# Performance work log

Hardware: AMD Instinct MI355X
Metric: run time of the kernel (lower is better)

Reference implementation:

```python
import jax, jax.numpy as jnp
import numpy as np

N_NODES = 50000
N_EDGES = 800000
N_GRAPHS = 256


def setup_inputs() -> dict:
    key = jax.random.key(0)
    ks = jax.random.split(key, 20)
    s = 0.05
    return {
        "x": jax.random.normal(ks[0], (N_NODES, 128), jnp.float32),
        "edge_index": jax.random.randint(ks[1], (2, N_EDGES), 0, N_NODES, jnp.int64),
        "batch_index": jnp.sort(jax.random.randint(ks[2], (N_NODES,), 0, N_GRAPHS, jnp.int64)),
        "mol_features": jax.random.normal(ks[3], (N_GRAPHS, 256), jnp.float32),
        "gcn_W": jax.random.normal(ks[4], (3, 128, 128), jnp.float32) * s,
        "gcn_b": jax.random.normal(ks[5], (3, 128), jnp.float32) * s,
        "gcn_out_W": jax.random.normal(ks[6], (128, 128), jnp.float32) * s,
        "gcn_out_b": jax.random.normal(ks[7], (128,), jnp.float32) * s,
        "mlp_W": jax.random.normal(ks[8], (2, 256, 256), jnp.float32) * s,
        "mlp_b": jax.random.normal(ks[9], (2, 256), jnp.float32) * s,
        "mlp_out_W": jax.random.normal(ks[10], (64, 256), jnp.float32) * s,
        "mlp_out_b": jax.random.normal(ks[11], (64,), jnp.float32) * s,
        "pred_W1": jax.random.normal(ks[12], (256, 192), jnp.float32) * s,
        "pred_b1": jax.random.normal(ks[13], (256,), jnp.float32) * s,
        "pred_W2": jax.random.normal(ks[14], (256, 256), jnp.float32) * s,
        "pred_b2": jax.random.normal(ks[15], (256,), jnp.float32) * s,
        "out_W": jax.random.normal(ks[16], (1, 256), jnp.float32) * s,
        "out_b": jax.random.normal(ks[17], (1,), jnp.float32) * s,
    }


def reference(x, edge_index, batch_index, mol_features,
              gcn_W, gcn_b, gcn_out_W, gcn_out_b,
              mlp_W, mlp_b, mlp_out_W, mlp_out_b,
              pred_W1, pred_b1, pred_W2, pred_b2, out_W, out_b):
    N = x.shape[0]
    E = edge_index.shape[1]
    G = mol_features.shape[0]
    row, col = edge_index[0], edge_index[1]

    # GCN normalization with self-loops (PyG gcn_norm, symmetric):
    # deg[i] = in-degree(i) + 1 (self loop); norm_e = d^-1/2[row] * d^-1/2[col]
    deg = jax.ops.segment_sum(jnp.ones((E,), x.dtype), col, num_segments=N) + 1.0
    dinv = jax.lax.rsqrt(deg)
    enorm = (dinv[row] * dinv[col])[:, None]     # [E,1]
    self_c = (dinv * dinv)[:, None]              # [N,1] self-loop coefficient

    h1 = x
    for i in range(gcn_W.shape[0]):
        h = h1 @ gcn_W[i].T                      # per-node transform [N,128]
        agg = jax.ops.segment_sum(h[row] * enorm, col, num_segments=N)
        h1 = jax.nn.relu(agg + self_c * h + gcn_b[i])
    h1 = h1 @ gcn_out_W.T + gcn_out_b            # final GCN-branch Linear (no relu)

    # global_mean_pool over batch_index -> [G,128]
    sums = jax.ops.segment_sum(h1, batch_index, num_segments=G)
    counts = jax.ops.segment_sum(jnp.ones((N,), x.dtype), batch_index, num_segments=G)
    h1 = sums / jnp.maximum(counts, 1.0)[:, None]

    # MLP branch: relu after every linear (including last)
    h2 = mol_features
    for i in range(mlp_W.shape[0]):
        h2 = jax.nn.relu(h2 @ mlp_W[i].T + mlp_b[i])
    h2 = jax.nn.relu(h2 @ mlp_out_W.T + mlp_out_b)

    h = jnp.concatenate([h1, h2], axis=1)        # [G,192]
    h = jax.nn.relu(h @ pred_W1.T + pred_b1)
    h = jax.nn.relu(h @ pred_W2.T + pred_b2)
    return h @ out_W.T + out_b                   # [G,1]
```

## Files before the change

kernel.cpp:

```cpp
#include <hip/hip_runtime.h>


typedef __attribute__((ext_vector_type(8))) short short8;
typedef __attribute__((ext_vector_type(4))) float f32x4;

#define BKT 64
#define SL 16
#define CAP 192
#define WCAP 2560
#define NBINBLK 2048
#define HROWS 65536

#define HW_MLP0 0
#define HW_MLP1 65536
#define HW_MLO  131072
#define HW_GCNO 147456
#define HW_PW1  163840
#define HW_PW2  212992
#define HW_TOT  278528

__device__ __forceinline__ unsigned short f2bf(float f) {
    union { float f; unsigned u; } c; c.f = f;
    unsigned u = c.u;
    unsigned r = u + 0x7FFFu + ((u >> 16) & 1u);
    return (unsigned short)(r >> 16);
}
__device__ __forceinline__ float bflo(unsigned w) {
    union { unsigned u; float f; } c; c.u = w << 16; return c.f;
}
__device__ __forceinline__ float bfhi(unsigned w) {
    union { unsigned u; float f; } c; c.u = w & 0xFFFF0000u; return c.f;
}

__global__ void k_init(int* cur, float* pool, float* cnt,
                       const float* __restrict__ gcnW, uint4* __restrict__ Wb,
                       const float* __restrict__ mlpW, const float* __restrict__ mloW,
                       const float* __restrict__ gcnoW, const float* __restrict__ pW1,
                       const float* __restrict__ pW2, unsigned short* __restrict__ Wh,
                       unsigned short* xb, unsigned short* bufA, unsigned short* bufB,
                       const int* __restrict__ batch, int M, int G, int N) {
    int i = blockIdx.x * 256 + threadIdx.x;
    if (i < M * 16) cur[i] = 0;
    if (i < G * 128) pool[i] = 0.f;
    if (i < G) {
        int lo = 0, hi = N;
        while (lo < hi) { int m = (lo + hi) >> 1; if (batch[m] < i) lo = m + 1; else hi = m; }
        int lo2 = lo, hi2 = N;
        while (lo2 < hi2) { int m = (lo2 + hi2) >> 1; if (batch[m] < i + 1) lo2 = m + 1; else hi2 = m; }
        cnt[i] = (float)(lo2 - lo);
    }
    if (i < 192) {
        unsigned short* b = (i < 64) ? xb : (i < 128) ? bufA : bufB;
        *(unsigned*)(b + (size_t)N * 128 + (i & 63) * 2) = 0u;
    }
    if (i < 3 * 2048) {
        int l = i >> 11, rem = i & 2047;
        int o = rem >> 4, c = rem & 15;
        const float4* s = (const float4*)(gcnW + (size_t)l * 16384 + o * 128 + c * 8);
        float4 a = s[0], b = s[1];
        uint4 v;
        v.x = ((unsigned)f2bf(a.y) << 16) | f2bf(a.x);
        v.y = ((unsigned)f2bf(a.w) << 16) | f2bf(a.z);
        v.z = ((unsigned)f2bf(b.y) << 16) | f2bf(b.x);
        v.w = ((unsigned)f2bf(b.w) << 16) | f2bf(b.z);
        Wb[(l << 11) | (o << 4) | (c ^ (o & 15))] = v;
    }
    int j = i - 8192;
    if (j >= 0 && j < (HW_TOT / 8)) {
        int e = j * 8;
        const float* src;
        if (e < HW_MLO)        src = mlpW  + e;
        else if (e < HW_GCNO)  src = mloW  + (e - HW_MLO);
        else if (e < HW_PW1)   src = gcnoW + (e - HW_GCNO);
        else if (e < HW_PW2)   src = pW1   + (e - HW_PW1);
        else                   src = pW2   + (e - HW_PW2);
        float4 a = *(const float4*)src;
        float4 b = *((const float4*)src + 1);
        uint4 v;
        v.x = ((unsigned)f2bf(a.y) << 16) | f2bf(a.x);
        v.y = ((unsigned)f2bf(a.w) << 16) | f2bf(a.z);
        v.z = ((unsigned)f2bf(b.y) << 16) | f2bf(b.x);
        v.w = ((unsigned)f2bf(b.w) << 16) | f2bf(b.z);
        *(uint4*)(Wh + e) = v;
    }
}

__global__ __launch_bounds__(256) void k_bin(const int* __restrict__ row,
                                             const int* __restrict__ col,
                                             int* __restrict__ cur,
                                             unsigned* __restrict__ gbin,
                                             int E, int C) {
    const int x = blockIdx.x & (SL - 1);
    int e0 = blockIdx.x * C, e1 = min(E, e0 + C);
    for (int e = e0 + threadIdx.x; e < e1; e += 256) {
        int c = col[e];
        int cell = (c >> 6) * SL + x;
        int cnt = atomicAdd(&cur[cell << 4], 1);
        gbin[cell * CAP + cnt] = (unsigned)row[e] | ((unsigned)(c & 63) << 16);
    }
}

__global__ __launch_bounds__(256) void k_csr(const unsigned* __restrict__ gbin,
                                             const int* __restrict__ cur,
                                             int* __restrict__ rs,
                                             unsigned short* __restrict__ rd,
                                             float* __restrict__ dinv,
                                             unsigned short* __restrict__ csrf,
                                             const float* __restrict__ x,
                                             unsigned short* __restrict__ xb,
                                             int N) {
    const int b = blockIdx.x, t = threadIdx.x;
    __shared__ int hcnt[64], lcur[64], fills[SL];
    __shared__ float sdinv[64];
    if (t < 64) hcnt[t] = 0;
    if (t < SL) fills[t] = cur[(b * SL + t) << 4];
    __syncthreads();
    #pragma unroll 4
    for (int xx = 0; xx < SL; ++xx) {
        int cbase = (b * SL + xx) * CAP, fill = fills[xx];
        for (int i = t; i < fill; i += 256)
            atomicAdd(&hcnt[(gbin[cbase + i] >> 16) & 63], 1);
    }
    __syncthreads();
    if (t < 64) {
        int v = hcnt[t];
        int vp = (v + 7) & ~7;
        int xs = vp;
        #pragma unroll
        for (int off = 1; off < 64; off <<= 1) {
            int u = __shfl_up(xs, off, 64);
            if (t >= off) xs += u;
        }
        int excl = xs - vp;
        lcur[t] = excl;
        float d = rsqrtf((float)v + 1.0f);
        sdinv[t] = d;
        int node = b * 64 + t;
        rs[node] = b * WCAP + excl;
        rd[node] = (unsigned short)v;
        dinv[node] = d;
    }
    __syncthreads();
    #pragma unroll 4
    for (int xx = 0; xx < SL; ++xx) {
        int cbase = (b * SL + xx) * CAP, fill = fills[xx];
        for (int i = t; i < fill; i += 256) {
            unsigned v = gbin[cbase + i];
            int p = atomicAdd(&lcur[(v >> 16) & 63], 1);
            csrf[b * WCAP + p] = (unsigned short)(v & 0xFFFFu);
        }
    }
    __syncthreads();
    if (t < 64) {
        int v = hcnt[t], vp = (v + 7) & ~7;
        int base = lcur[t];
        for (int p = v; p < vp; ++p)
            csrf[b * WCAP + base + (p - v)] = (unsigned short)N;
    }
    const int node0 = b * 64;
    #pragma unroll
    for (int it = 0; it < 4; ++it) {
        int i = t + it * 256;
        int nd = node0 + (i >> 4);
        if (nd < N) {
            int ch = i & 15;
            float d = sdinv[i >> 4];
            const float4* s = (const float4*)(x + (size_t)nd * 128 + ch * 8);
            float4 a = s[0], bb = s[1];
            uint4 o;
            o.x = ((unsigned)f2bf(d * a.y) << 16) | f2bf(d * a.x);
            o.y = ((unsigned)f2bf(d * a.w) << 16) | f2bf(d * a.z);
            o.z = ((unsigned)f2bf(d * bb.y) << 16) | f2bf(d * bb.x);
            o.w = ((unsigned)f2bf(d * bb.w) << 16) | f2bf(d * bb.z);
            *(uint4*)(xb + (size_t)nd * 128 + ch * 8) = o;
        }
    }
}

__global__ __launch_bounds__(1024, 8) void k_fused(
    const unsigned short* __restrict__ h,
    const uint4* __restrict__ Wb,
    const float* __restrict__ bias,
    const float* __restrict__ dscale,
    const float* __restrict__ dinv,
    const int* __restrict__ rs,
    const unsigned short* __restrict__ rd,
    const unsigned short* __restrict__ csrf,
    unsigned short* __restrict__ C,
    const int* __restrict__ batch,
    float* __restrict__ pool, int N) {
    __shared__ uint4 Wsh[2048];
    __shared__ unsigned short Ash[64][136];
    __shared__ unsigned short Ish[WCAP];

    const int t = threadIdx.x;
    Wsh[t] = Wb[t];
    Wsh[t + 1024] = Wb[t + 1024];

    const int sub = t >> 4;
    const int fg = t & 15;
    const int blk0 = blockIdx.x * 64;
    const int node = blk0 + sub;

    const int base = blockIdx.x * WCAP;
    const int ln = blk0 + 63;
    const int wcnt = (rs[ln] + ((rd[ln] + 7) & ~7)) - base;
    for (int i = t * 8; i < wcnt; i += 8192)
        *(uint4*)(&Ish[i]) = *(const uint4*)(csrf + base + i);
    __syncthreads();

    float acc[8] = {0.f, 0.f, 0.f, 0.f, 0.f, 0.f, 0.f, 0.f};
    const unsigned fgo = (unsigned)fg * 8u;
    if (node < N) {
        uint4 hv = *(const uint4*)(h + (size_t)node * 128u + fgo);
        acc[0] = bflo(hv.x); acc[1] = bfhi(hv.x);
        acc[2] = bflo(hv.y); acc[3] = bfhi(hv.y);
        acc[4] = bflo(hv.z); acc[5] = bfhi(hv.z);
        acc[6] = bflo(hv.w); acc[7] = bfhi(hv.w);
    }
    {
        const int stl = rs[node] - base;
        const int epl = stl + ((rd[node] + 7) & ~7);
        #pragma unroll 1
        for (int i = stl; i < epl; i += 4) {
            const uint2 iv = *(const uint2*)(&Ish[i]);
            const uint4 v0 = *(const uint4*)(h + ((iv.x & 0xFFFFu) * 128u + fgo));
            const uint4 v1 = *(const uint4*)(h + ((iv.x >> 16)     * 128u + fgo));
            const uint4 v2 = *(const uint4*)(h + ((iv.y & 0xFFFFu) * 128u + fgo));
            const uint4 v3 = *(const uint4*)(h + ((iv.y >> 16)     * 128u + fgo));
            acc[0] += bflo(v0.x); acc[1] += bfhi(v0.x);
            acc[2] += bflo(v0.y); acc[3] += bfhi(v0.y);
            acc[4] += bflo(v0.z); acc[5] += bfhi(v0.z);
            acc[6] += bflo(v0.w); acc[7] += bfhi(v0.w);
            acc[0] += bflo(v1.x); acc[1] += bfhi(v1.x);
            acc[2] += bflo(v1.y); acc[3] += bfhi(v1.y);
            acc[4] += bflo(v1.z); acc[5] += bfhi(v1.z);
            acc[6] += bflo(v1.w); acc[7] += bfhi(v1.w);
            acc[0] += bflo(v2.x); acc[1] += bfhi(v2.x);
            acc[2] += bflo(v2.y); acc[3] += bfhi(v2.y);
            acc[4] += bflo(v2.z); acc[5] += bfhi(v2.z);
            acc[6] += bflo(v2.w); acc[7] += bfhi(v2.w);
            acc[0] += bflo(v3.x); acc[1] += bfhi(v3.x);
            acc[2] += bflo(v3.y); acc[3] += bfhi(v3.y);
            acc[4] += bflo(v3.z); acc[5] += bfhi(v3.z);
            acc[6] += bflo(v3.w); acc[7] += bfhi(v3.w);
        }
    }
    {
        const float dn = (node < N) ? dinv[node] : 0.f;
        unsigned short ob[8];
        #pragma unroll
        for (int j = 0; j < 8; ++j) ob[j] = f2bf(acc[j] * dn);
        uint4 o;
        o.x = ((unsigned)ob[1] << 16) | ob[0];
        o.y = ((unsigned)ob[3] << 16) | ob[2];
        o.z = ((unsigned)ob[5] << 16) | ob[4];
        o.w = ((unsigned)ob[7] << 16) | ob[6];
        *(uint4*)(&Ash[sub][fg * 8]) = o;
    }
    __syncthreads();

    const int lane = t & 63;
    const int wv = t >> 6;
    const int l15 = lane & 15, quad = lane >> 4;
    const int rt = wv & 3, cp = wv >> 2;
    f32x4 acc2[2];
    acc2[0] = (f32x4){0.f, 0.f, 0.f, 0.f};
    acc2[1] = (f32x4){0.f, 0.f, 0.f, 0.f};
    #pragma unroll
    for (int kiter = 0; kiter < 4; ++kiter) {
        short8 af = *(const short8*)(&Ash[rt * 16 + l15][kiter * 32 + quad * 8]);
        const int cswz = (kiter * 4 + quad) ^ l15;
        #pragma unroll
        for (int cc = 0; cc < 2; ++cc) {
            int ct = cp * 2 + cc;
            short8 bf = *(const short8*)(&Wsh[((ct * 16 + l15) << 4) | cswz]);
            acc2[cc] = __builtin_amdgcn_mfma_f32_16x16x32_bf16(af, bf, acc2[cc], 0, 0, 0);
        }
    }

    const int rbase = blk0 + rt * 16 + quad * 4;
    if (pool) {
        int gr[4];
        #pragma unroll
        for (int r = 0; r < 4; ++r)
            gr[r] = (rbase + r < N) ? batch[rbase + r] : -1;
        #pragma unroll
        for (int cc = 0; cc < 2; ++cc) {
            int colc = (cp * 2 + cc) * 16 + l15;
            float bcol = bias[colc];
            float s = 0.f; int gprev = -2;
            #pragma unroll
            for (int r = 0; r < 4; ++r) {
                if (gr[r] >= 0) {
                    float v = fmaxf(acc2[cc][r] + bcol, 0.f);
                    if (gr[r] == gprev) s += v;
                    else {
                        if (gprev >= 0) atomicAdd(&pool[(size_t)gprev * 128 + colc], s);
                        gprev = gr[r]; s = v;
                    }
                }
            }
            if (gprev >= 0) atomicAdd(&pool[(size_t)gprev * 128 + colc], s);
        }
    } else {
        float ds[4];
        #pragma unroll
        for (int r = 0; r < 4; ++r) {
            int rr = rbase + r;
            ds[r] = (dscale && rr < N) ? dscale[rr] : 1.f;
        }
        #pragma unroll
        for (int cc = 0; cc < 2; ++cc) {
            int colc = (cp * 2 + cc) * 16 + l15;
            float bcol = bias[colc];
            #pragma unroll
            for (int r = 0; r < 4; ++r) {
                int rr = rbase + r;
                if (rr < N) {
                    float v = fmaxf(acc2[cc][r] + bcol, 0.f) * ds[r];
                    C[(size_t)rr * 128 + colc] = f2bf(v);
                }
            }
        }
    }
}

__global__ __launch_bounds__(256) void k_head(
    const unsigned short* __restrict__ Wh,
    const float* __restrict__ pool, const float* __restrict__ cnt,
    const float* __restrict__ mol,
    const float* __restrict__ mlpb, const float* __restrict__ mlob,
    const float* __restrict__ gcnob,
    const float* __restrict__ pb1, const float* __restrict__ pb2,
    const float* __restrict__ oW, const float* __restrict__ ob,
    float* __restrict__ out, int G) {
    const int g0 = blockIdx.x * 16;
    const int t = threadIdx.x;
    const int lane = t & 63, wv = t >> 6;
    const int l15 = lane & 15, quad = lane >> 4;
    __shared__ unsigned short A[16][264], B[16][264], Cc[16][200], Mn[16][136];
    __shared__ float red[4][16];

    for (int i = t; i < 16 * 256; i += 256) {
        int g = i >> 8, k = i & 255;
        A[g][k] = f2bf(mol[(size_t)(g0 + g) * 256 + k]);
    }
    for (int i = t; i < 16 * 128; i += 256) {
        int g = i >> 7, k = i & 127;
        float c = cnt[g0 + g];
        Mn[g][k] = f2bf(pool[(size_t)(g0 + g) * 128 + k] / fmaxf(c, 1.f));
    }
    __syncthreads();

    auto do_tile = [&](const unsigned short* actb, int astr, int K,
                       const unsigned short* W, int orow,
                       const float* __restrict__ bias, int bidx,
                       unsigned short* dstb, int dstr, int ocol, bool dorelu) {
        f32x4 c = {0.f, 0.f, 0.f, 0.f};
        for (int kt = 0; kt < (K >> 5); ++kt) {
            short8 af = *(const short8*)(actb + (size_t)l15 * astr + kt * 32 + quad * 8);
            short8 bf = *(const short8*)(W + (size_t)orow * K + kt * 32 + quad * 8);
            c = __builtin_amdgcn_mfma_f32_16x16x32_bf16(af, bf, c, 0, 0, 0);
        }
        float bb = bias[bidx];
        #pragma unroll
        for (int r = 0; r < 4; ++r) {
            int g = quad * 4 + r;
            float v = c[r] + bb;
            if (dorelu) v = fmaxf(v, 0.f);
            dstb[(size_t)g * dstr + ocol] = f2bf(v);
        }
    };

    #pragma unroll
    for (int nt = 0; nt < 4; ++nt) {
        int o = (wv * 4 + nt) * 16 + l15;
        do_tile(&A[0][0], 264, 256, Wh + HW_MLP0, o, mlpb, o, &B[0][0], 264, o, true);
    }
    __syncthreads();
    #pragma unroll
    for (int nt = 0; nt < 4; ++nt) {
        int o = (wv * 4 + nt) * 16 + l15;
        do_tile(&B[0][0], 264, 256, Wh + HW_MLP1, o, mlpb + 256, o, &A[0][0], 264, o, true);
    }
    __syncthreads();
    #pragma unroll
    for (int j = 0; j < 3; ++j) {
        int tile = wv * 3 + j;
        if (tile < 8) {
            int o = tile * 16 + l15;
            do_tile(&Mn[0][0], 136, 128, Wh + HW_GCNO, o, gcnob, o, &Cc[0][0], 200, o, false);
        } else {
            int om = (tile - 8) * 16 + l15;
            do_tile(&A[0][0], 264, 256, Wh + HW_MLO, om, mlob, om, &Cc[0][0], 200, 128 + om, true);
        }
    }
    __syncthreads();
    #pragma unroll
    for (int nt = 0; nt < 4; ++nt) {
        int o = (wv * 4 + nt) * 16 + l15;
        do_tile(&Cc[0][0], 200, 192, Wh + HW_PW1, o, pb1, o, &B[0][0], 264, o, true);
    }
    __syncthreads();
    {
        float pacc[4] = {0.f, 0.f, 0.f, 0.f};
        #pragma unroll
        for (int nt = 0; nt < 4; ++nt) {
            int o = (wv * 4 + nt) * 16 + l15;
            f32x4 c = {0.f, 0.f, 0.f, 0.f};
            #pragma unroll
            for (int kt = 0; kt < 8; ++kt) {
                short8 af = *(const short8*)(&B[0][0] + (size_t)l15 * 264 + kt * 32 + quad * 8);
                short8 bf = *(const short8*)(Wh + HW_PW2 + (size_t)o * 256 + kt * 32 + quad * 8);
                c = __builtin_amdgcn_mfma_f32_16x16x32_bf16(af, bf, c, 0, 0, 0);
            }
            float bb = pb2[o], wo = oW[o];
            #pragma unroll
            for (int r = 0; r < 4; ++r)
                pacc[r] += fmaxf(c[r] + bb, 0.f) * wo;
        }
        #pragma unroll
        for (int off = 1; off < 16; off <<= 1)
            #pragma unroll
            for (int r = 0; r < 4; ++r)
                pacc[r] += __shfl_xor(pacc[r], off, 64);
        if (l15 == 0) {
            #pragma unroll
            for (int r = 0; r < 4; ++r)
                red[wv][quad * 4 + r] = pacc[r];
        }
    }
    __syncthreads();
    if (t < 16) {
        float s = red[0][t] + red[1][t] + red[2][t] + red[3][t] + ob[0];
        if (g0 + t < G) out[g0 + t] = s;
    }
}

extern "C" void kernel_launch(void* const* d_in, const int* in_sizes, int n_in,
                              void* d_out, int out_size, void* d_ws, size_t ws_size,
                              hipStream_t stream) {
    const float* x     = (const float*)d_in[0];
    const int*   ei    = (const int*)d_in[1];
    const int*   batch = (const int*)d_in[2];
    const float* mol   = (const float*)d_in[3];
    const float* gcnW  = (const float*)d_in[4];
    const float* gcnb  = (const float*)d_in[5];
    const float* gcnoW = (const float*)d_in[6];
    const float* gcnob = (const float*)d_in[7];
    const float* mlpW  = (const float*)d_in[8];
    const float* mlpb  = (const float*)d_in[9];
    const float* mloW  = (const float*)d_in[10];
    const float* mlob  = (const float*)d_in[11];
    const float* pW1   = (const float*)d_in[12];
    const float* pb1   = (const float*)d_in[13];
    const float* pW2   = (const float*)d_in[14];
    const float* pb2   = (const float*)d_in[15];
    const float* oW    = (const float*)d_in[16];
    const float* ob    = (const float*)d_in[17];

    const int N = in_sizes[0] / 128;
    const int E = in_sizes[1] / 2;
    const int G = in_sizes[3] / 256;
    const int* row = ei;
    const int* col = ei + E;

    const int NBK = (N + BKT - 1) / BKT;
    const int M = NBK * SL;
    const int C = (E + NBINBLK - 1) / NBINBLK;

    char* p = (char*)d_ws;
    auto alloc = [&](size_t bytes) {
        char* q = p;
        p += (bytes + 255) & ~(size_t)255;
        return (void*)q;
    };
    int*    rs    = (int*)alloc((size_t)NBK * 64 * 4);
    unsigned short* rd = (unsigned short*)alloc((size_t)NBK * 64 * 2);
    float*  dinv  = (float*)alloc((size_t)NBK * 64 * 4);
    int*    cur   = (int*)alloc((size_t)M * 16 * 4);
    unsigned* gbin = (unsigned*)alloc((size_t)M * CAP * 4);
    unsigned short* csrf = (unsigned short*)alloc(((size_t)NBK * WCAP + 32) * 2);
    unsigned short* xb   = (unsigned short*)alloc((size_t)HROWS * 128 * 2);
    unsigned short* bufA = (unsigned short*)alloc((size_t)HROWS * 128 * 2);
    unsigned short* bufB = (unsigned short*)alloc((size_t)HROWS * 128 * 2);
    uint4*  Wb    = (uint4*)alloc((size_t)3 * 2048 * 16);
    unsigned short* Wh = (unsigned short*)alloc((size_t)HW_TOT * 2);
    float*  pool  = (float*)alloc((size_t)G * 128 * 4);
    float*  cnt   = (float*)alloc((size_t)G * 4);

    const int initblocks = (M * 16 + 255) / 256;

    k_init<<<initblocks, 256, 0, stream>>>(cur, pool, cnt, gcnW, Wb,
                                           mlpW, mloW, gcnoW, pW1, pW2, Wh,
                                           xb, bufA, bufB, batch, M, G, N);
    k_bin<<<NBINBLK, 256, 0, stream>>>(row, col, cur, gbin, E, C);
    k_csr<<<NBK, 256, 0, stream>>>(gbin, cur, rs, rd, dinv, csrf, x, xb, N);

    const int fblocks = (N + 63) / 64;
    k_fused<<<fblocks, 1024, 0, stream>>>(xb, Wb, gcnb, dinv, dinv,
                                          rs, rd, csrf, bufA,
                                          batch, (float*)nullptr, N);
    k_fused<<<fblocks, 1024, 0, stream>>>(bufA, Wb + 2048, gcnb + 128, dinv, dinv,
                                          rs, rd, csrf, bufB,
                                          batch, (float*)nullptr, N);
    k_fused<<<fblocks, 1024, 0, stream>>>(bufB, Wb + 4096, gcnb + 256,
                                          (const float*)nullptr, dinv,
                                          rs, rd, csrf, bufA,
                                          batch, pool, N);
    k_head<<<(G + 15) / 16, 256, 0, stream>>>(
        Wh, pool, cnt, mol, mlpb, mlob, gcnob, pb1, pb2, oW, ob,
        (float*)d_out, G);
}
```

Baseline: 320.8 us.

## Merge all stages into one persistent cooperative kernel with grid syncs

Replaces the seven separate launches (init, bin, csr, three GCN layers, head) with one cooperative persistent kernel. Stages are separated by grid-wide syncs, and each stage uses grid-stride loops over tiles. The goal is to remove launch overhead and the gaps between kernels. In exchange, grid syncs add cost, the grid is capped at a few hundred blocks of 1024 threads, and stages with little work (csr, head) leave most threads idle.

```diff
diff --git a/kernel.cpp b/kernel.cpp
--- a/kernel.cpp
+++ b/kernel.cpp
@@ -1,4 +1,6 @@
 #include <hip/hip_runtime.h>
+#include <hip/hip_cooperative_groups.h>
+namespace cg = cooperative_groups;
 
 
 typedef __attribute__((ext_vector_type(8))) short short8;
@@ -8,7 +10,6 @@
 #define SL 16
 #define CAP 192
 #define WCAP 2560
-#define NBINBLK 2048
 #define HROWS 65536
 
 #define HW_MLP0 0
@@ -32,409 +33,415 @@
     union { unsigned u; float f; } c; c.u = w & 0xFFFF0000u; return c.f;
 }
 
-__global__ void k_init(int* cur, float* pool, float* cnt,
-                       const float* __restrict__ gcnW, uint4* __restrict__ Wb,
-                       const float* __restrict__ mlpW, const float* __restrict__ mloW,
-                       const float* __restrict__ gcnoW, const float* __restrict__ pW1,
-                       const float* __restrict__ pW2, unsigned short* __restrict__ Wh,
-                       unsigned short* xb, unsigned short* bufA, unsigned short* bufB,
-                       const int* __restrict__ batch, int M, int G, int N) {
-    int i = blockIdx.x * 256 + threadIdx.x;
-    if (i < M * 16) cur[i] = 0;
-    if (i < G * 128) pool[i] = 0.f;
-    if (i < G) {
-        int lo = 0, hi = N;
-        while (lo < hi) { int m = (lo + hi) >> 1; if (batch[m] < i) lo = m + 1; else hi = m; }
-        int lo2 = lo, hi2 = N;
-        while (lo2 < hi2) { int m = (lo2 + hi2) >> 1; if (batch[m] < i + 1) lo2 = m + 1; else hi2 = m; }
-        cnt[i] = (float)(lo2 - lo);
+struct MegaParams {
+    int* cur; float* pool; float* cnt;
+    const float* gcnW; uint4* Wb;
+    const float* mlpW; const float* mloW; const float* gcnoW;
+    const float* pW1; const float* pW2; unsigned short* Wh;
+    unsigned short* xb; unsigned short* bufA; unsigned short* bufB;
+    const int* batch; const int* row; const int* col;
+    unsigned* gbin;
+    int* rs; unsigned short* rd; float* dinv; unsigned short* csrf;
+    const float* x; const float* gcnb;
+    const float* mol; const float* mlpb; const float* mlob; const float* gcnob;
+    const float* pb1; const float* pb2; const float* oW; const float* ob;
+    float* out;
+    int M, G, N, E, NBK;
+};
+
+__global__ __launch_bounds__(1024, 8) void k_mega(MegaParams p) {
+    cg::grid_group gg = cg::this_grid();
+    const int t = threadIdx.x;
+    const int nb = gridDim.x;
+
+    union SMem {
+        struct { uint4 Wsh[2048]; unsigned short Ash[64][136];
+                 unsigned short Ish[WCAP]; } f;
+        struct { int hcnt[64]; int lcur[64]; int fills[SL];
+                 float sdinv[64]; } c;
+        struct { unsigned short A[16][264]; unsigned short Bs[16][264];
+                 unsigned short Cc[16][200]; unsigned short Mn[16][136];
+                 float red[4][16]; } h;
+    };
+    __shared__ SMem sm;
+
+    {
+        const int itot = p.M * 16;
+        for (int i = blockIdx.x * 1024 + t; i < itot; i += nb * 1024) {
+            p.cur[i] = 0;
+            if (i < p.G * 128) p.pool[i] = 0.f;
+            if (i < p.G) {
+                int lo = 0, hi = p.N;
+                while (lo < hi) { int m = (lo + hi) >> 1; if (p.batch[m] < i) lo = m + 1; else hi = m; }
+                int lo2 = lo, hi2 = p.N;
+                while (lo2 < hi2) { int m = (lo2 + hi2) >> 1; if (p.batch[m] < i + 1) lo2 = m + 1; else hi2 = m; }
+                p.cnt[i] = (float)(lo2 - lo);
+            }
+            if (i < 192) {
+                unsigned short* b = (i < 64) ? p.xb : (i < 128) ? p.bufA : p.bufB;
+                *(unsigned*)(b + (size_t)p.N * 128 + (i & 63) * 2) = 0u;
+            }
+            if (i < 3 * 2048) {
+                int l = i >> 11, rem = i & 2047;
+                int o = rem >> 4, c = rem & 15;
+                const float4* s = (const float4*)(p.gcnW + (size_t)l * 16384 + o * 128 + c * 8);
+                float4 a = s[0], b = s[1];
+                uint4 v;
+                v.x = ((unsigned)f2bf(a.y) << 16) | f2bf(a.x);
+                v.y = ((unsigned)f2bf(a.w) << 16) | f2bf(a.z);
+                v.z = ((unsigned)f2bf(b.y) << 16) | f2bf(b.x);
+                v.w = ((unsigned)f2bf(b.w) << 16) | f2bf(b.z);
+                p.Wb[(l << 11) | (o << 4) | (c ^ (o & 15))] = v;
+            }
+            int j = i - 8192;
+            if (j >= 0 && j < (HW_TOT / 8)) {
+                int e = j * 8;
+                const float* src;
+                if (e < HW_MLO)        src = p.mlpW  + e;
+                else if (e < HW_GCNO)  src = p.mloW  + (e - HW_MLO);
+                else if (e < HW_PW1)   src = p.gcnoW + (e - HW_GCNO);
+                else if (e < HW_PW2)   src = p.pW1   + (e - HW_PW1);
+                else                   src = p.pW2   + (e - HW_PW2);
+                float4 a = *(const float4*)src;
+                float4 b = *((const float4*)src + 1);
+                uint4 v;
+                v.x = ((unsigned)f2bf(a.y) << 16) | f2bf(a.x);
+                v.y = ((unsigned)f2bf(a.w) << 16) | f2bf(a.z);
+                v.z = ((unsigned)f2bf(b.y) << 16) | f2bf(b.x);
+                v.w = ((unsigned)f2bf(b.w) << 16) | f2bf(b.z);
+                *(uint4*)(p.Wh + e) = v;
+            }
+        }
     }
-    if (i < 192) {
-        unsigned short* b = (i < 64) ? xb : (i < 128) ? bufA : bufB;
-        *(unsigned*)(b + (size_t)N * 128 + (i & 63) * 2) = 0u;
+    gg.sync();
+
+    {
+        const int x = blockIdx.x & (SL - 1);
+        for (int e = blockIdx.x * 1024 + t; e < p.E; e += nb * 1024) {
+            int c = p.col[e];
+            int cell = (c >> 6) * SL + x;
+            int cnt = atomicAdd(&p.cur[cell << 4], 1);
+            p.gbin[cell * CAP + cnt] = (unsigned)p.row[e] | ((unsigned)(c & 63) << 16);
+        }
     }
-    if (i < 3 * 2048) {
-        int l = i >> 11, rem = i & 2047;
-        int o = rem >> 4, c = rem & 15;
-        const float4* s = (const float4*)(gcnW + (size_t)l * 16384 + o * 128 + c * 8);
-        float4 a = s[0], b = s[1];
-        uint4 v;
-        v.x = ((unsigned)f2bf(a.y) << 16) | f2bf(a.x);
-        v.y = ((unsigned)f2bf(a.w) << 16) | f2bf(a.z);
-        v.z = ((unsigned)f2bf(b.y) << 16) | f2bf(b.x);
-        v.w = ((unsigned)f2bf(b.w) << 16) | f2bf(b.z);
-        Wb[(l << 11) | (o << 4) | (c ^ (o & 15))] = v;
+    gg.sync();
+
+    for (int b = blockIdx.x; b < p.NBK; b += nb) {
+        if (t < 64) sm.c.hcnt[t] = 0;
+        if (t < SL) sm.c.fills[t] = p.cur[(b * SL + t) << 4];
+        __syncthreads();
+        for (int xx = 0; xx < SL; ++xx) {
+            int cbase = (b * SL + xx) * CAP, fill = sm.c.fills[xx];
+            for (int i = t; i < fill; i += 1024)
+                atomicAdd(&sm.c.hcnt[(p.gbin[cbase + i] >> 16) & 63], 1);
+        }
+        __syncthreads();
+        if (t < 64) {
+            int v = sm.c.hcnt[t];
+            int vp = (v + 7) & ~7;
+            int xs = vp;
+            #pragma unroll
+            for (int off = 1; off < 64; off <<= 1) {
+                int u = __shfl_up(xs, off, 64);
+                if (t >= off) xs += u;
+            }
+            int excl = xs - vp;
+            sm.c.lcur[t] = excl;
+            float d = rsqrtf((float)v + 1.0f);
+            sm.c.sdinv[t] = d;
+            int node = b * 64 + t;
+            p.rs[node] = b * WCAP + excl;
+            p.rd[node] = (unsigned short)v;
+            p.dinv[node] = d;
+        }
+        __syncthreads();
+        for (int xx = 0; xx < SL; ++xx) {
+            int cbase = (b * SL + xx) * CAP, fill = sm.c.fills[xx];
+            for (int i = t; i < fill; i += 1024) {
+                unsigned v = p.gbin[cbase + i];
+                int pp = atomicAdd(&sm.c.lcur[(v >> 16) & 63], 1);
+                p.csrf[b * WCAP + pp] = (unsigned short)(v & 0xFFFFu);
+            }
+        }
+        __syncthreads();
+        if (t < 64) {
+            int v = sm.c.hcnt[t], vp = (v + 7) & ~7;
+            int base = sm.c.lcur[t];
+            for (int q = v; q < vp; ++q)
+                p.csrf[b * WCAP + base + (q - v)] = (unsigned short)p.N;
+        }
+        {
+            int nd = b * 64 + (t >> 4);
+            if (nd < p.N) {
+                int ch = t & 15;
+                float d = sm.c.sdinv[t >> 4];
+                const float4* s = (const float4*)(p.x + (size_t)nd * 128 + ch * 8);
+                float4 a = s[0], bb = s[1];
+                uint4 o;
+                o.x = ((unsigned)f2bf(d * a.y) << 16) | f2bf(d * a.x);
+                o.y = ((unsigned)f2bf(d * a.w) << 16) | f2bf(d * a.z);
+                o.z = ((unsigned)f2bf(d * bb.y) << 16) | f2bf(d * bb.x);
+                o.w = ((unsigned)f2bf(d * bb.w) << 16) | f2bf(d * bb.z);
+                *(uint4*)(p.xb + (size_t)nd * 128 + ch * 8) = o;
+            }
+        }
+        __syncthreads();
     }
-    int j = i - 8192;
-    if (j >= 0 && j < (HW_TOT / 8)) {
-        int e = j * 8;
-        const float* src;
-        if (e < HW_MLO)        src = mlpW  + e;
-        else if (e < HW_GCNO)  src = mloW  + (e - HW_MLO);
-        else if (e < HW_PW1)   src = gcnoW + (e - HW_GCNO);
-        else if (e < HW_PW2)   src = pW1   + (e - HW_PW1);
-        else                   src = pW2   + (e - HW_PW2);
-        float4 a = *(const float4*)src;
-        float4 b = *((const float4*)src + 1);
-        uint4 v;
-        v.x = ((unsigned)f2bf(a.y) << 16) | f2bf(a.x);
-        v.y = ((unsigned)f2bf(a.w) << 16) | f2bf(a.z);
-        v.z = ((unsigned)f2bf(b.y) << 16) | f2bf(b.x);
-        v.w = ((unsigned)f2bf(b.w) << 16) | f2bf(b.z);
-        *(uint4*)(Wh + e) = v;
+    gg.sync();
+
+    {
+        const int sub = t >> 4;
+        const int fg = t & 15;
+        const unsigned fgo = (unsigned)fg * 8u;
+        const int fblocks = (p.N + 63) / 64;
+        for (int l = 0; l < 3; ++l) {
+            const unsigned short* h = (l == 0) ? p.xb : (l == 1) ? p.bufA : p.bufB;
+            unsigned short* Cd = (l == 0) ? p.bufA : p.bufB;
+            const float* dscale = (l < 2) ? p.dinv : (const float*)nullptr;
+            float* pl = (l == 2) ? p.pool : (float*)nullptr;
+            const float* bias = p.gcnb + l * 128;
+            const uint4* Wbl = p.Wb + l * 2048;
+            sm.f.Wsh[t] = Wbl[t];
+            sm.f.Wsh[t + 1024] = Wbl[t + 1024];
+
+            for (int tile = blockIdx.x; tile < fblocks; tile += nb) {
+                __syncthreads();
+                const int blk0 = tile * 64;
+                const int node = blk0 + sub;
+                const int base = tile * WCAP;
+                const int ln = blk0 + 63;
+                const int wcnt = (p.rs[ln] + ((p.rd[ln] + 7) & ~7)) - base;
+                for (int i = t * 8; i < wcnt; i += 8192)
+                    *(uint4*)(&sm.f.Ish[i]) = *(const uint4*)(p.csrf + base + i);
+                __syncthreads();
+
+                float acc[8] = {0.f, 0.f, 0.f, 0.f, 0.f, 0.f, 0.f, 0.f};
+                if (node < p.N) {
+                    uint4 hv = *(const uint4*)(h + (size_t)node * 128u + fgo);
+                    acc[0] = bflo(hv.x); acc[1] = bfhi(hv.x);
+                    acc[2] = bflo(hv.y); acc[3] = bfhi(hv.y);
+                    acc[4] = bflo(hv.z); acc[5] = bfhi(hv.z);
+                    acc[6] = bflo(hv.w); acc[7] = bfhi(hv.w);
+                }
+                {
+                    const int stl = p.rs[node] - base;
+                    const int epl = stl + ((p.rd[node] + 7) & ~7);
+                    #pragma unroll 1
+                    for (int i = stl; i < epl; i += 4) {
+                        const uint2 iv = *(const uint2*)(&sm.f.Ish[i]);
+                        const uint4 v0 = *(const uint4*)(h + ((iv.x & 0xFFFFu) * 128u + fgo));
+                        const uint4 v1 = *(const uint4*)(h + ((iv.x >> 16)     * 128u + fgo));
+                        const uint4 v2 = *(const uint4*)(h + ((iv.y & 0xFFFFu) * 128u + fgo));
+                        const uint4 v3 = *(const uint4*)(h + ((iv.y >> 16)     * 128u + fgo));
+                        acc[0] += bflo(v0.x); acc[1] += bfhi(v0.x);
+                        acc[2] += bflo(v0.y); acc[3] += bfhi(v0.y);
+                        acc[4] += bflo(v0.z); acc[5] += bfhi(v0.z);
+                        acc[6] += bflo(v0.w); acc[7] += bfhi(v0.w);
+                        acc[0] += bflo(v1.x); acc[1] += bfhi(v1.x);
+                        acc[2] += bflo(v1.y); acc[3] += bfhi(v1.y);
+                        acc[4] += bflo(v1.z); acc[5] += bfhi(v1.z);
+                        acc[6] += bflo(v1.w); acc[7] += bfhi(v1.w);
+                        acc[0] += bflo(v2.x); acc[1] += bfhi(v2.x);
+                        acc[2] += bflo(v2.y); acc[3] += bfhi(v2.y);
+                        acc[4] += bflo(v2.z); acc[5] += bfhi(v2.z);
+                        acc[6] += bflo(v2.w); acc[7] += bfhi(v2.w);
+                        acc[0] += bflo(v3.x); acc[1] += bfhi(v3.x);
+                        acc[2] += bflo(v3.y); acc[3] += bfhi(v3.y);
+                        acc[4] += bflo(v3.z); acc[5] += bfhi(v3.z);
+                        acc[6] += bflo(v3.w); acc[7] += bfhi(v3.w);
+                    }
+                }
+                {
+                    const float dn = (node < p.N) ? p.dinv[node] : 0.f;
+                    unsigned short ob[8];
+                    #pragma unroll
+                    for (int j = 0; j < 8; ++j) ob[j] = f2bf(acc[j] * dn);
+                    uint4 o;
+                    o.x = ((unsigned)ob[1] << 16) | ob[0];
+                    o.y = ((unsigned)ob[3] << 16) | ob[2];
+                    o.z = ((unsigned)ob[5] << 16) | ob[4];
+                    o.w = ((unsigned)ob[7] << 16) | ob[6];
+                    *(uint4*)(&sm.f.Ash[sub][fg * 8]) = o;
+                }
+                __syncthreads();
+
+                const int lane = t & 63;
+                const int wv = t >> 6;
+                const int l15 = lane & 15, quad = lane >> 4;
+                const int rt = wv & 3, cp = wv >> 2;
+                f32x4 acc2[2];
+                acc2[0] = (f32x4){0.f, 0.f, 0.f, 0.f};
+                acc2[1] = (f32x4){0.f, 0.f, 0.f, 0.f};
+                #pragma unroll
+                for (int kiter = 0; kiter < 4; ++kiter) {
+                    short8 af = *(const short8*)(&sm.f.Ash[rt * 16 + l15][kiter * 32 + quad * 8]);
+                    const int cswz = (kiter * 4 + quad) ^ l15;
+                    #pragma unroll
+                    for (int cc = 0; cc < 2; ++cc) {
+                        int ct = cp * 2 + cc;
+                        short8 bf = *(const short8*)(&sm.f.Wsh[((ct * 16 + l15) << 4) | cswz]);
+                        acc2[cc] = __builtin_amdgcn_mfma_f32_16x16x32_bf16(af, bf, acc2[cc], 0, 0, 0);
+                    }
+                }
+                const int rbase = blk0 + rt * 16 + quad * 4;
+                if (pl) {
+                    int gr[4];
+                    #pragma unroll
+                    for (int r = 0; r < 4; ++r)
+                        gr[r] = (rbase + r < p.N) ? p.batch[rbase + r] : -1;
+                    #pragma unroll
+                    for (int cc = 0; cc < 2; ++cc) {
+                        int colc = (cp * 2 + cc) * 16 + l15;
+                        float bcol = bias[colc];
+                        float s = 0.f; int gprev = -2;
+                        #pragma unroll
+                        for (int r = 0; r < 4; ++r) {
+                            if (gr[r] >= 0) {
+                                float v = fmaxf(acc2[cc][r] + bcol, 0.f);
+                                if (gr[r] == gprev) s += v;
+                                else {
+                                    if (gprev >= 0) atomicAdd(&pl[(size_t)gprev * 128 + colc], s);
+                                    gprev = gr[r]; s = v;
+                                }
+                            }
+                        }
+                        if (gprev >= 0) atomicAdd(&pl[(size_t)gprev * 128 + colc], s);
+                    }
+                } else {
+                    float ds[4];
+                    #pragma unroll
+                    for (int r = 0; r < 4; ++r) {
+                        int rr = rbase + r;
+                        ds[r] = (dscale && rr < p.N) ? dscale[rr] : 1.f;
+                    }
+                    #pragma unroll
+                    for (int cc = 0; cc < 2; ++cc) {
+                        int colc = (cp * 2 + cc) * 16 + l15;
+                        float bcol = bias[colc];
+                        #pragma unroll
+                        for (int r = 0; r < 4; ++r) {
+                            int rr = rbase + r;
+                            if (rr < p.N) {
+                                float v = fmaxf(acc2[cc][r] + bcol, 0.f) * ds[r];
+                                Cd[(size_t)rr * 128 + colc] = f2bf(v);
+                            }
+                        }
+                    }
+                }
+            }
+            gg.sync();
+        }
     }
-}
-
-__global__ __launch_bounds__(256) void k_bin(const int* __restrict__ row,
-                                             const int* __restrict__ col,
-                                             int* __restrict__ cur,
-                                             unsigned* __restrict__ gbin,
-                                             int E, int C) {
-    const int x = blockIdx.x & (SL - 1);
-    int e0 = blockIdx.x * C, e1 = min(E, e0 + C);
-    for (int e = e0 + threadIdx.x; e < e1; e += 256) {
-        int c = col[e];
-        int cell = (c >> 6) * SL + x;
-        int cnt = atomicAdd(&cur[cell << 4], 1);
-        gbin[cell * CAP + cnt] = (unsigned)row[e] | ((unsigned)(c & 63) << 16);
-    }
-}
-
-__global__ __launch_bounds__(256) void k_csr(const unsigned* __restrict__ gbin,
-                                             const int* __restrict__ cur,
-                                             int* __restrict__ rs,
-                                             unsigned short* __restrict__ rd,
-                                             float* __restrict__ dinv,
-                                             unsigned short* __restrict__ csrf,
-                                             const float* __restrict__ x,
-                                             unsigned short* __restrict__ xb,
-                                             int N) {
-    const int b = blockIdx.x, t = threadIdx.x;
-    __shared__ int hcnt[64], lcur[64], fills[SL];
-    __shared__ float sdinv[64];
-    if (t < 64) hcnt[t] = 0;
-    if (t < SL) fills[t] = cur[(b * SL + t) << 4];
-    __syncthreads();
-    #pragma unroll 4
-    for (int xx = 0; xx < SL; ++xx) {
-        int cbase = (b * SL + xx) * CAP, fill = fills[xx];
-        for (int i = t; i < fill; i += 256)
-            atomicAdd(&hcnt[(gbin[cbase + i] >> 16) & 63], 1);
-    }
-    __syncthreads();
-    if (t < 64) {
-        int v = hcnt[t];
-        int vp = (v + 7) & ~7;
-        int xs = vp;
-        #pragma unroll
-        for (int off = 1; off < 64; off <<= 1) {
-            int u = __shfl_up(xs, off, 64);
-            if (t >= off) xs += u;
-        }
-        int excl = xs - vp;
-        lcur[t] = excl;
-        float d = rsqrtf((float)v + 1.0f);
-        sdinv[t] = d;
-        int node = b * 64 + t;
-        rs[node] = b * WCAP + excl;
-        rd[node] = (unsigned short)v;
-        dinv[node] = d;
-    }
-    __syncthreads();
-    #pragma unroll 4
-    for (int xx = 0; xx < SL; ++xx) {
-        int cbase = (b * SL + xx) * CAP, fill = fills[xx];
-        for (int i = t; i < fill; i += 256) {
-            unsigned v = gbin[cbase + i];
-            int p = atomicAdd(&lcur[(v >> 16) & 63], 1);
-            csrf[b * WCAP + p] = (unsigned short)(v & 0xFFFFu);
-        }
-    }
-    __syncthreads();
-    if (t < 64) {
-        int v = hcnt[t], vp = (v + 7) & ~7;
-        int base = lcur[t];
-        for (int p = v; p < vp; ++p)
-            csrf[b * WCAP + base + (p - v)] = (unsigned short)N;
-    }
-    const int node0 = b * 64;
-    #pragma unroll
-    for (int it = 0; it < 4; ++it) {
-        int i = t + it * 256;
-        int nd = node0 + (i >> 4);
-        if (nd < N) {
-            int ch = i & 15;
-            float d = sdinv[i >> 4];
-            const float4* s = (const float4*)(x + (size_t)nd * 128 + ch * 8);
-            float4 a = s[0], bb = s[1];
-            uint4 o;
-            o.x = ((unsigned)f2bf(d * a.y) << 16) | f2bf(d * a.x);
-            o.y = ((unsigned)f2bf(d * a.w) << 16) | f2bf(d * a.z);
-            o.z = ((unsigned)f2bf(d * bb.y) << 16) | f2bf(d * bb.x);
-            o.w = ((unsigned)f2bf(d * bb.w) << 16) | f2bf(d * bb.z);
-            *(uint4*)(xb + (size_t)nd * 128 + ch * 8) = o;
-        }
-    }
-}
-
-__global__ __launch_bounds__(1024, 8) void k_fused(
-    const unsigned short* __restrict__ h,
-    const uint4* __restrict__ Wb,
-    const float* __restrict__ bias,
-    const float* __restrict__ dscale,
-    const float* __restrict__ dinv,
-    const int* __restrict__ rs,
-    const unsigned short* __restrict__ rd,
-    const unsigned short* __restrict__ csrf,
-    unsigned short* __restrict__ C,
-    const int* __restrict__ batch,
-    float* __restrict__ pool, int N) {
-    __shared__ uint4 Wsh[2048];
-    __shared__ unsigned short Ash[64][136];
-    __shared__ unsigned short Ish[WCAP];
-
-    const int t = threadIdx.x;
-    Wsh[t] = Wb[t];
-    Wsh[t + 1024] = Wb[t + 1024];
-
-    const int sub = t >> 4;
-    const int fg = t & 15;
-    const int blk0 = blockIdx.x * 64;
-    const int node = blk0 + sub;
-
-    const int base = blockIdx.x * WCAP;
-    const int ln = blk0 + 63;
-    const int wcnt = (rs[ln] + ((rd[ln] + 7) & ~7)) - base;
-    for (int i = t * 8; i < wcnt; i += 8192)
-        *(uint4*)(&Ish[i]) = *(const uint4*)(csrf + base + i);
-    __syncthreads();
-
-    float acc[8] = {0.f, 0.f, 0.f, 0.f, 0.f, 0.f, 0.f, 0.f};
-    const unsigned fgo = (unsigned)fg * 8u;
-    if (node < N) {
-        uint4 hv = *(const uint4*)(h + (size_t)node * 128u + fgo);
-        acc[0] = bflo(hv.x); acc[1] = bfhi(hv.x);
-        acc[2] = bflo(hv.y); acc[3] = bfhi(hv.y);
-        acc[4] = bflo(hv.z); acc[5] = bfhi(hv.z);
-        acc[6] = bflo(hv.w); acc[7] = bfhi(hv.w);
-    }
-    {
-        const int stl = rs[node] - base;
-        const int epl = stl + ((rd[node] + 7) & ~7);
-        #pragma unroll 1
-        for (int i = stl; i < epl; i += 4) {
-            const uint2 iv = *(const uint2*)(&Ish[i]);
-            const uint4 v0 = *(const uint4*)(h + ((iv.x & 0xFFFFu) * 128u + fgo));
-            const uint4 v1 = *(const uint4*)(h + ((iv.x >> 16)     * 128u + fgo));
-            const uint4 v2 = *(const uint4*)(h + ((iv.y & 0xFFFFu) * 128u + fgo));
-            const uint4 v3 = *(const uint4*)(h + ((iv.y >> 16)     * 128u + fgo));
-            acc[0] += bflo(v0.x); acc[1] += bfhi(v0.x);
-            acc[2] += bflo(v0.y); acc[3] += bfhi(v0.y);
-            acc[4] += bflo(v0.z); acc[5] += bfhi(v0.z);
-            acc[6] += bflo(v0.w); acc[7] += bfhi(v0.w);
-            acc[0] += bflo(v1.x); acc[1] += bfhi(v1.x);
-            acc[2] += bflo(v1.y); acc[3] += bfhi(v1.y);
-            acc[4] += bflo(v1.z); acc[5] += bfhi(v1.z);
-            acc[6] += bflo(v1.w); acc[7] += bfhi(v1.w);
-            acc[0] += bflo(v2.x); acc[1] += bfhi(v2.x);
-            acc[2] += bflo(v2.y); acc[3] += bfhi(v2.y);
-            acc[4] += bflo(v2.z); acc[5] += bfhi(v2.z);
-            acc[6] += bflo(v2.w); acc[7] += bfhi(v2.w);
-            acc[0] += bflo(v3.x); acc[1] += bfhi(v3.x);
-            acc[2] += bflo(v3.y); acc[3] += bfhi(v3.y);
-            acc[4] += bflo(v3.z); acc[5] += bfhi(v3.z);
-            acc[6] += bflo(v3.w); acc[7] += bfhi(v3.w);
-        }
-    }
-    {
-        const float dn = (node < N) ? dinv[node] : 0.f;
-        unsigned short ob[8];
-        #pragma unroll
-        for (int j = 0; j < 8; ++j) ob[j] = f2bf(acc[j] * dn);
-        uint4 o;
-        o.x = ((unsigned)ob[1] << 16) | ob[0];
-        o.y = ((unsigned)ob[3] << 16) | ob[2];
-        o.z = ((unsigned)ob[5] << 16) | ob[4];
-        o.w = ((unsigned)ob[7] << 16) | ob[6];
-        *(uint4*)(&Ash[sub][fg * 8]) = o;
-    }
-    __syncthreads();
-
-    const int lane = t & 63;
-    const int wv = t >> 6;
-    const int l15 = lane & 15, quad = lane >> 4;
-    const int rt = wv & 3, cp = wv >> 2;
-    f32x4 acc2[2];
-    acc2[0] = (f32x4){0.f, 0.f, 0.f, 0.f};
-    acc2[1] = (f32x4){0.f, 0.f, 0.f, 0.f};
-    #pragma unroll
-    for (int kiter = 0; kiter < 4; ++kiter) {
-        short8 af = *(const short8*)(&Ash[rt * 16 + l15][kiter * 32 + quad * 8]);
-        const int cswz = (kiter * 4 + quad) ^ l15;
-        #pragma unroll
-        for (int cc = 0; cc < 2; ++cc) {
-            int ct = cp * 2 + cc;
-            short8 bf = *(const short8*)(&Wsh[((ct * 16 + l15) << 4) | cswz]);
-            acc2[cc] = __builtin_amdgcn_mfma_f32_16x16x32_bf16(af, bf, acc2[cc], 0, 0, 0);
-        }
-    }
-
-    const int rbase = blk0 + rt * 16 + quad * 4;
-    if (pool) {
-        int gr[4];
-        #pragma unroll
-        for (int r = 0; r < 4; ++r)
-            gr[r] = (rbase + r < N) ? batch[rbase + r] : -1;
-        #pragma unroll
-        for (int cc = 0; cc < 2; ++cc) {
-            int colc = (cp * 2 + cc) * 16 + l15;
-            float bcol = bias[colc];
-            float s = 0.f; int gprev = -2;
+
+    if (blockIdx.x < (p.G + 15) / 16) {
+        const int g0 = blockIdx.x * 16;
+        const int lane = t & 63, wv = t >> 6;
+        const int l15 = lane & 15, quad = lane >> 4;
+
+        if (t < 256) {
+            for (int i = t; i < 16 * 256; i += 256) {
+                int g = i >> 8, k = i & 255;
+                sm.h.A[g][k] = f2bf(p.mol[(size_t)(g0 + g) * 256 + k]);
+            }
+            for (int i = t; i < 16 * 128; i += 256) {
+                int g = i >> 7, k = i & 127;
+                float c = p.cnt[g0 + g];
+                sm.h.Mn[g][k] = f2bf(p.pool[(size_t)(g0 + g) * 128 + k] / fmaxf(c, 1.f));
+            }
+        }
+        __syncthreads();
+
+        auto do_tile = [&](const unsigned short* actb, int astr, int K,
+                           const unsigned short* W, int orow,
+                           const float* __restrict__ bias, int bidx,
+                           unsigned short* dstb, int dstr, int ocol, bool dorelu) {
+            f32x4 c = {0.f, 0.f, 0.f, 0.f};
+            for (int kt = 0; kt < (K >> 5); ++kt) {
+                short8 af = *(const short8*)(actb + (size_t)l15 * astr + kt * 32 + quad * 8);
+                short8 bf = *(const short8*)(W + (size_t)orow * K + kt * 32 + quad * 8);
+                c = __builtin_amdgcn_mfma_f32_16x16x32_bf16(af, bf, c, 0, 0, 0);
+            }
+            float bb = bias[bidx];
             #pragma unroll
             for (int r = 0; r < 4; ++r) {
-                if (gr[r] >= 0) {
-                    float v = fmaxf(acc2[cc][r] + bcol, 0.f);
-                    if (gr[r] == gprev) s += v;
-                    else {
-                        if (gprev >= 0) atomicAdd(&pool[(size_t)gprev * 128 + colc], s);
-                        gprev = gr[r]; s = v;
-                    }
-                }
-            }
-            if (gprev >= 0) atomicAdd(&pool[(size_t)gprev * 128 + colc], s);
-        }
-    } else {
-        float ds[4];
-        #pragma unroll
-        for (int r = 0; r < 4; ++r) {
-            int rr = rbase + r;
-            ds[r] = (dscale && rr < N) ? dscale[rr] : 1.f;
-        }
-        #pragma unroll
-        for (int cc = 0; cc < 2; ++cc) {
-            int colc = (cp * 2 + cc) * 16 + l15;
-            float bcol = bias[colc];
-            #pragma unroll
-            for (int r = 0; r < 4; ++r) {
-                int rr = rbase + r;
-                if (rr < N) {
-                    float v = fmaxf(acc2[cc][r] + bcol, 0.f) * ds[r];
-                    C[(size_t)rr * 128 + colc] = f2bf(v);
-                }
-            }
-        }
-    }
-}
-
-__global__ __launch_bounds__(256) void k_head(
-    const unsigned short* __restrict__ Wh,
-    const float* __restrict__ pool, const float* __restrict__ cnt,
-    const float* __restrict__ mol,
-    const float* __restrict__ mlpb, const float* __restrict__ mlob,
-    const float* __restrict__ gcnob,
-    const float* __restrict__ pb1, const float* __restrict__ pb2,
-    const float* __restrict__ oW, const float* __restrict__ ob,
-    float* __restrict__ out, int G) {
-    const int g0 = blockIdx.x * 16;
-    const int t = threadIdx.x;
-    const int lane = t & 63, wv = t >> 6;
-    const int l15 = lane & 15, quad = lane >> 4;
-    __shared__ unsigned short A[16][264], B[16][264], Cc[16][200], Mn[16][136];
-    __shared__ float red[4][16];
-
-    for (int i = t; i < 16 * 256; i += 256) {
-        int g = i >> 8, k = i & 255;
-        A[g][k] = f2bf(mol[(size_t)(g0 + g) * 256 + k]);
-    }
-    for (int i = t; i < 16 * 128; i += 256) {
-        int g = i >> 7, k = i & 127;
-        float c = cnt[g0 + g];
-        Mn[g][k] = f2bf(pool[(size_t)(g0 + g) * 128 + k] / fmaxf(c, 1.f));
-    }
-    __syncthreads();
-
-    auto do_tile = [&](const unsigned short* actb, int astr, int K,
-                       const unsigned short* W, int orow,
-                       const float* __restrict__ bias, int bidx,
-                       unsigned short* dstb, int dstr, int ocol, bool dorelu) {
-        f32x4 c = {0.f, 0.f, 0.f, 0.f};
-        for (int kt = 0; kt < (K >> 5); ++kt) {
-            short8 af = *(const short8*)(actb + (size_t)l15 * astr + kt * 32 + quad * 8);
-            short8 bf = *(const short8*)(W + (size_t)orow * K + kt * 32 + quad * 8);
-            c = __builtin_amdgcn_mfma_f32_16x16x32_bf16(af, bf, c, 0, 0, 0);
-        }
-        float bb = bias[bidx];
-        #pragma unroll
-        for (int r = 0; r < 4; ++r) {
-            int g = quad * 4 + r;
-            float v = c[r] + bb;
-            if (dorelu) v = fmaxf(v, 0.f);
-            dstb[(size_t)g * dstr + ocol] = f2bf(v);
-        }
-    };
-
-    #pragma unroll
-    for (int nt = 0; nt < 4; ++nt) {
-        int o = (wv * 4 + nt) * 16 + l15;
-        do_tile(&A[0][0], 264, 256, Wh + HW_MLP0, o, mlpb, o, &B[0][0], 264, o, true);
-    }
-    __syncthreads();
-    #pragma unroll
-    for (int nt = 0; nt < 4; ++nt) {
-        int o = (wv * 4 + nt) * 16 + l15;
-        do_tile(&B[0][0], 264, 256, Wh + HW_MLP1, o, mlpb + 256, o, &A[0][0], 264, o, true);
-    }
-    __syncthreads();
-    #pragma unroll
-    for (int j = 0; j < 3; ++j) {
-        int tile = wv * 3 + j;
-        if (tile < 8) {
-            int o = tile * 16 + l15;
-            do_tile(&Mn[0][0], 136, 128, Wh + HW_GCNO, o, gcnob, o, &Cc[0][0], 200, o, false);
-        } else {
-            int om = (tile - 8) * 16 + l15;
-            do_tile(&A[0][0], 264, 256, Wh + HW_MLO, om, mlob, om, &Cc[0][0], 200, 128 + om, true);
-        }
-    }
-    __syncthreads();
-    #pragma unroll
-    for (int nt = 0; nt < 4; ++nt) {
-        int o = (wv * 4 + nt) * 16 + l15;
-        do_tile(&Cc[0][0], 200, 192, Wh + HW_PW1, o, pb1, o, &B[0][0], 264, o, true);
-    }
-    __syncthreads();
-    {
-        float pacc[4] = {0.f, 0.f, 0.f, 0.f};
-        #pragma unroll
-        for (int nt = 0; nt < 4; ++nt) {
-            int o = (wv * 4 + nt) * 16 + l15;
-            f32x4 c = {0.f, 0.f, 0.f, 0.f};
-            #pragma unroll
-            for (int kt = 0; kt < 8; ++kt) {
-                short8 af = *(const short8*)(&B[0][0] + (size_t)l15 * 264 + kt * 32 + quad * 8);
-                short8 bf = *(const short8*)(Wh + HW_PW2 + (size_t)o * 256 + kt * 32 + quad * 8);
-                c = __builtin_amdgcn_mfma_f32_16x16x32_bf16(af, bf, c, 0, 0, 0);
-            }
-            float bb = pb2[o], wo = oW[o];
-            #pragma unroll
-            for (int r = 0; r < 4; ++r)
-                pacc[r] += fmaxf(c[r] + bb, 0.f) * wo;
-        }
-        #pragma unroll
-        for (int off = 1; off < 16; off <<= 1)
-            #pragma unroll
-            for (int r = 0; r < 4; ++r)
-                pacc[r] += __shfl_xor(pacc[r], off, 64);
-        if (l15 == 0) {
-            #pragma unroll
-            for (int r = 0; r < 4; ++r)
-                red[wv][quad * 4 + r] = pacc[r];
-        }
-    }
-    __syncthreads();
-    if (t < 16) {
-        float s = red[0][t] + red[1][t] + red[2][t] + red[3][t] + ob[0];
-        if (g0 + t < G) out[g0 + t] = s;
+                int g = quad * 4 + r;
+                float v = c[r] + bb;
+                if (dorelu) v = fmaxf(v, 0.f);
+                dstb[(size_t)g * dstr + ocol] = f2bf(v);
+            }
+        };
+
+        if (t < 256) {
+            #pragma unroll
+            for (int nt = 0; nt < 4; ++nt) {
+                int o = (wv * 4 + nt) * 16 + l15;
+                do_tile(&sm.h.A[0][0], 264, 256, p.Wh + HW_MLP0, o, p.mlpb, o, &sm.h.Bs[0][0], 264, o, true);
+            }
+        }
+        __syncthreads();
+        if (t < 256) {
+            #pragma unroll
+            for (int nt = 0; nt < 4; ++nt) {
+                int o = (wv * 4 + nt) * 16 + l15;
+                do_tile(&sm.h.Bs[0][0], 264, 256, p.Wh + HW_MLP1, o, p.mlpb + 256, o, &sm.h.A[0][0], 264, o, true);
+            }
+        }
+        __syncthreads();
+        if (t < 256) {
+            #pragma unroll
+            for (int j = 0; j < 3; ++j) {
+                int tile = wv * 3 + j;
+                if (tile < 8) {
+                    int o = tile * 16 + l15;
+                    do_tile(&sm.h.Mn[0][0], 136, 128, p.Wh + HW_GCNO, o, p.gcnob, o, &sm.h.Cc[0][0], 200, o, false);
+                } else {
+                    int om = (tile - 8) * 16 + l15;
+                    do_tile(&sm.h.A[0][0], 264, 256, p.Wh + HW_MLO, om, p.mlob, om, &sm.h.Cc[0][0], 200, 128 + om, true);
+                }
+            }
+        }
+        __syncthreads();
+        if (t < 256) {
+            #pragma unroll
+            for (int nt = 0; nt < 4; ++nt) {
+                int o = (wv * 4 + nt) * 16 + l15;
+                do_tile(&sm.h.Cc[0][0], 200, 192, p.Wh + HW_PW1, o, p.pb1, o, &sm.h.Bs[0][0], 264, o, true);
+            }
+        }
+        __syncthreads();
+        if (t < 256) {
+            float pacc[4] = {0.f, 0.f, 0.f, 0.f};
+            #pragma unroll
+            for (int nt = 0; nt < 4; ++nt) {
+                int o = (wv * 4 + nt) * 16 + l15;
+                f32x4 c = {0.f, 0.f, 0.f, 0.f};
+                #pragma unroll
+                for (int kt = 0; kt < 8; ++kt) {
+                    short8 af = *(const short8*)(&sm.h.Bs[0][0] + (size_t)l15 * 264 + kt * 32 + quad * 8);
+                    short8 bf = *(const short8*)(p.Wh + HW_PW2 + (size_t)o * 256 + kt * 32 + quad * 8);
+                    c = __builtin_amdgcn_mfma_f32_16x16x32_bf16(af, bf, c, 0, 0, 0);
+                }
+                float bb = p.pb2[o], wo = p.oW[o];
+                #pragma unroll
+                for (int r = 0; r < 4; ++r)
+                    pacc[r] += fmaxf(c[r] + bb, 0.f) * wo;
+            }
+            #pragma unroll
+            for (int off = 1; off < 16; off <<= 1)
+                #pragma unroll
+                for (int r = 0; r < 4; ++r)
+                    pacc[r] += __shfl_xor(pacc[r], off, 64);
+            if (l15 == 0) {
+                #pragma unroll
+                for (int r = 0; r < 4; ++r)
+                    sm.h.red[wv][quad * 4 + r] = pacc[r];
+            }
+        }
+        __syncthreads();
+        if (t < 16) {
+            float s = sm.h.red[0][t] + sm.h.red[1][t] + sm.h.red[2][t] + sm.h.red[3][t] + p.ob[0];
+            if (g0 + t < p.G) p.out[g0 + t] = s;
+        }
     }
 }
 
@@ -468,7 +475,6 @@
 
     const int NBK = (N + BKT - 1) / BKT;
     const int M = NBK * SL;
-    const int C = (E + NBINBLK - 1) / NBINBLK;
 
     char* p = (char*)d_ws;
     auto alloc = [&](size_t bytes) {
@@ -490,26 +496,27 @@
     float*  pool  = (float*)alloc((size_t)G * 128 * 4);
     float*  cnt   = (float*)alloc((size_t)G * 4);
 
-    const int initblocks = (M * 16 + 255) / 256;
-
-    k_init<<<initblocks, 256, 0, stream>>>(cur, pool, cnt, gcnW, Wb,
-                                           mlpW, mloW, gcnoW, pW1, pW2, Wh,
-                                           xb, bufA, bufB, batch, M, G, N);
-    k_bin<<<NBINBLK, 256, 0, stream>>>(row, col, cur, gbin, E, C);
-    k_csr<<<NBK, 256, 0, stream>>>(gbin, cur, rs, rd, dinv, csrf, x, xb, N);
-
-    const int fblocks = (N + 63) / 64;
-    k_fused<<<fblocks, 1024, 0, stream>>>(xb, Wb, gcnb, dinv, dinv,
-                                          rs, rd, csrf, bufA,
-                                          batch, (float*)nullptr, N);
-    k_fused<<<fblocks, 1024, 0, stream>>>(bufA, Wb + 2048, gcnb + 128, dinv, dinv,
-                                          rs, rd, csrf, bufB,
-                                          batch, (float*)nullptr, N);
-    k_fused<<<fblocks, 1024, 0, stream>>>(bufB, Wb + 4096, gcnb + 256,
-                                          (const float*)nullptr, dinv,
-                                          rs, rd, csrf, bufA,
-                                          batch, pool, N);
-    k_head<<<(G + 15) / 16, 256, 0, stream>>>(
-        Wh, pool, cnt, mol, mlpb, mlob, gcnob, pb1, pb2, oW, ob,
-        (float*)d_out, G);
+    MegaParams mp;
+    mp.cur = cur; mp.pool = pool; mp.cnt = cnt;
+    mp.gcnW = gcnW; mp.Wb = Wb;
+    mp.mlpW = mlpW; mp.mloW = mloW; mp.gcnoW = gcnoW;
+    mp.pW1 = pW1; mp.pW2 = pW2; mp.Wh = Wh;
+    mp.xb = xb; mp.bufA = bufA; mp.bufB = bufB;
+    mp.batch = batch; mp.row = row; mp.col = col;
+    mp.gbin = gbin;
+    mp.rs = rs; mp.rd = rd; mp.dinv = dinv; mp.csrf = csrf;
+    mp.x = x; mp.gcnb = gcnb;
+    mp.mol = mol; mp.mlpb = mlpb; mp.mlob = mlob; mp.gcnob = gcnob;
+    mp.pb1 = pb1; mp.pb2 = pb2; mp.oW = oW; mp.ob = ob;
+    mp.out = (float*)d_out;
+    mp.M = M; mp.G = G; mp.N = N; mp.E = E; mp.NBK = NBK;
+
+    int perCU = 0;
+    hipOccupancyMaxActiveBlocksPerMultiprocessor(&perCU, k_mega, 1024, 0);
+    if (perCU < 1) perCU = 1;
+    int nb = perCU * 256;
+    if (nb > 512) nb = 512;
+
+    void* args[] = { &mp };
+    hipLaunchCooperativeKernel((void*)k_mega, dim3(nb), dim3(1024), args, 0, stream);
 }
```

After: 574.9 us. 1.79x slower.
